# Optimization experiments

Measured on AMD Instinct MI355X. Metric: run time of the kernel, lower is better.

## Reference

```python
import jax, jax.numpy as jnp
import numpy as np

B, T, C, H = 2, 64, 384, 768
LR, MOM, DECAY = 0.01, 0.9, 0.001


def pscan(gates, tokens):
    """parallel_scan_log: x[t] = gates[t]*x[t-1] + tokens[t] along axis 1.
    gates [B,S], tokens [B,S,...]."""
    extra = tokens.ndim - gates.ndim
    g = gates.reshape(gates.shape + (1,) * extra)
    g = jnp.clip(g, 1e-7, 1.0 - 1e-7)
    lc = jnp.cumsum(jnp.log(g), axis=1)              # log cumulative gates
    return jnp.exp(lc) * jnp.cumsum(tokens * jnp.exp(-lc), axis=1)


def setup_inputs():
    key = jax.random.key(0)
    ks = jax.random.split(key, 12)
    s = 0.02
    W0 = jax.random.normal(ks[0], (H, C), jnp.float32) * s
    W1 = jax.random.normal(ks[1], (C, H), jnp.float32) * s
    return {
        "x": jax.random.normal(ks[2], (B, T, C), jnp.float32),
        "Wq": jax.random.normal(ks[3], (C, C), jnp.float32) * s, "bq": jnp.zeros((C,), jnp.float32),
        "Wk": jax.random.normal(ks[4], (C, C), jnp.float32) * s, "bk": jnp.zeros((C,), jnp.float32),
        "Wv": jax.random.normal(ks[5], (C, C), jnp.float32) * s, "bv": jnp.zeros((C,), jnp.float32),
        "Wo": jax.random.normal(ks[6], (C, C), jnp.float32) * s, "bo": jnp.zeros((C,), jnp.float32),
        "init_query": jax.random.normal(ks[7], (1, 1, C), jnp.float32) * s,
        "sW0": jnp.broadcast_to(W0, (B, H, C)) + 0.0,
        "sb0": jnp.zeros((B, H), jnp.float32),
        "sW1": jnp.broadcast_to(W1, (B, C, H)) + 0.0,
        "sb1": jnp.zeros((B, C), jnp.float32),
    }


def reference(x, Wq, bq, Wk, bk, Wv, bv, Wo, bo, init_query, sW0, sb0, sW1, sb1):
    dt = x.dtype
    # ---- retrieval (causal: uses init_query since no previous segment) ----
    q = jnp.broadcast_to(init_query, (B, 1, C)) @ Wq.T + bq          # [B,1,C]
    h_pre = jnp.einsum('bqc,bhc->bqh', q, sW0) + sb0[:, None]
    h = h_pre * jax.nn.sigmoid(h_pre)                                 # SiLU
    pred = jnp.einsum('bqh,bch->bqc', h, sW1) + sb1[:, None]
    out = pred @ Wo.T + bo                                            # [B,1,C]

    # ---- test-time memory update: per-token MSE gradients ----
    k = x @ Wk.T + bk                                                 # [B,T,C]
    v = x @ Wv.T + bv
    h1_pre = jnp.einsum('btc,bhc->bth', k, sW0) + sb0[:, None]
    sig = jax.nn.sigmoid(h1_pre)
    h1 = h1_pre * sig
    p = jnp.einsum('bth,bch->btc', h1, sW1) + sb1[:, None]
    dp = p - v                                                        # d(MSE)/d(pred)
    dW1 = jnp.einsum('btc,bth->btch', dp, h1)                         # [B,T,C,H]
    db1 = dp
    dh1 = jnp.einsum('btc,bch->bth', dp, sW1)
    dh1p = dh1 * (sig * (1 + h1_pre * (1 - sig)))                     # SiLU grad
    dW0 = jnp.einsum('bth,btc->bthc', dh1p, k)                        # [B,T,H,C]
    db0 = dh1p

    # ---- momentum scan + decayed weight scan ----
    def update(W, g):
        surprise = -LR * g                                            # [B,T,...]
        m = pscan(jnp.full((B, T), MOM, dt), (1.0 - MOM) * surprise)  # EMA of surprises
        toks = jnp.concatenate([W[:, None], m], axis=1)               # seed with current weight
        gts = jnp.concatenate([jnp.ones((B, 1), dt),
                               jnp.full((B, T), 1.0 - DECAY, dt)], axis=1)
        return pscan(gts, toks)[:, -1]                                # final weight after segment

    nW0 = update(sW0, dW0)
    nb0 = update(sb0, db0)
    nW1 = update(sW1, dW1)
    nb1 = update(sb1, db1)
    return out, nW0, nb0, nW1, nb1
```

## Files before the change

### kernel.cpp

```cpp
#include <hip/hip_runtime.h>
#include <hip/hip_bf16.h>
#include <cmath>

#define BB 2
#define TT 64
#define CC 384
#define HH 768

#define O_OUT 0
#define O_NW0 768
#define O_NB0 (768 + 589824)
#define O_NW1 (O_NB0 + 1536)
#define O_NB1 (O_NW1 + 589824)

#define GRID_BLKS 312
#define BAR_MAGIC 0x5F3A9D71u
#define AGT __HIP_MEMORY_SCOPE_AGENT

#define W_ARRX(w, x) (32 + ((w) * 8 + (x)) * 32)
#define W_WBD(w)     (1056 + (w) * 32)
#define W_DONE(w)    (1184 + (w) * 32)
#define W_DEP        1312
#define W_NJAN       1344
#define W_CLAIM      1376
#define BAR_WORDS    1536

struct Coefs { float ct[TT]; float dfac; };

typedef __attribute__((ext_vector_type(8))) short bf16x8;
typedef __attribute__((ext_vector_type(4))) float f32x4;

__device__ __forceinline__ float bf2f(unsigned short u) {
    union { unsigned int i; float f; } x; x.i = ((unsigned int)u) << 16; return x.f;
}
__device__ __forceinline__ unsigned short f2bf(float f) {
    union { float f; unsigned int i; } u; u.f = f;
    unsigned int x = u.i;
    unsigned int r = (x + 0x7fffu + ((x >> 16) & 1u)) >> 16;
    return (unsigned short)r;
}
__device__ __forceinline__ f32x4 mfma16(bf16x8 a, bf16x8 b, f32x4 c) {
    return __builtin_amdgcn_mfma_f32_16x16x32_bf16(a, b, c, 0, 0, 0);
}
__device__ __forceinline__ bf16x8 ldbf8(const unsigned short* p) {
    return *(const bf16x8*)p;
}
__device__ __forceinline__ bf16x8 ldcvt8(const float* p) {
    float4 a = *(const float4*)p, b = *(const float4*)(p + 4);
    bf16x8 r;
    r[0] = (short)f2bf(a.x); r[1] = (short)f2bf(a.y); r[2] = (short)f2bf(a.z); r[3] = (short)f2bf(a.w);
    r[4] = (short)f2bf(b.x); r[5] = (short)f2bf(b.y); r[6] = (short)f2bf(b.z); r[7] = (short)f2bf(b.w);
    return r;
}

__device__ __forceinline__ unsigned aload(unsigned* p) {
    return __hip_atomic_load(p, __ATOMIC_RELAXED, AGT);
}
__device__ __forceinline__ void aadd(unsigned* p, unsigned v) {
    __hip_atomic_fetch_add(p, v, __ATOMIC_RELAXED, AGT);
}
__device__ __forceinline__ void astore(unsigned* p, unsigned v) {
    __hip_atomic_store(p, v, __ATOMIC_RELAXED, AGT);
}
__device__ __forceinline__ void bar_reset(unsigned* bar) {
    for (int i = 0; i < 32; ++i) astore(bar + 32 + i * 32, 0u);
    for (int w = 0; w < 4; ++w) { astore(bar + W_WBD(w), 0u); astore(bar + W_DONE(w), 0u); }
    astore(bar + W_DEP, 0u);
    astore(bar + W_NJAN, 0u);
    for (int i = 0; i < 8; ++i) astore(bar + W_CLAIM + i, 0u);
}

struct KArgs {
    const float *x, *Wq, *bq, *Wk, *bk, *Wv, *bv, *Wo, *bo, *iq;
    const float *sW0, *sb0, *sW1, *sb1;
    unsigned short *kb_bf, *h1_bf, *dp_bf;
    float *vb, *qb, *hret, *pred, *dsil, *dh1p, *warm;
    unsigned *bar;
    float *out;
    Coefs cf;
};

__device__ __forceinline__ void gsync(unsigned* bar, int w, bool jan, int xcc) {
    __syncthreads();
    if (threadIdx.x == 0) {
        aadd(bar + W_ARRX(w, xcc), 1u);
        if (jan) {
            for (;;) {
                unsigned s = 0;
                #pragma unroll
                for (int x = 0; x < 8; ++x) s += aload(bar + W_ARRX(w, x));
                if (s == GRID_BLKS) break;
                __builtin_amdgcn_s_sleep(2);
            }
            __builtin_amdgcn_fence(__ATOMIC_RELEASE, "agent");
            asm volatile("s_waitcnt vmcnt(0)" ::: "memory");
            aadd(bar + W_WBD(w), 1u);
            unsigned nj = aload(bar + W_NJAN);
            while (aload(bar + W_WBD(w)) < nj) __builtin_amdgcn_s_sleep(2);
            __builtin_amdgcn_fence(__ATOMIC_ACQUIRE, "agent");
            aadd(bar + W_DONE(w), 1u);
        }
        for (;;) {
            unsigned d = aload(bar + W_DONE(w));
            if (d) { unsigned nj = aload(bar + W_NJAN); if (d >= nj) break; }
            __builtin_amdgcn_s_sleep(2);
        }
        if (w == 3) {
            unsigned old = __hip_atomic_fetch_add(bar + W_DEP, 1u, __ATOMIC_RELAXED, AGT);
            if (old == GRID_BLKS - 1) bar_reset(bar);
        }
    }
    __syncthreads();
}

__global__ void __launch_bounds__(256, 2) fused(KArgs A) {
    __shared__ __align__(16) unsigned char sbuf[49920];
    const int blk = blockIdx.x, j = threadIdx.x;

    bool jan = false; int xcc = 0;
    if (j == 0) {
        if (blk == 0) {
            if (aload(A.bar) != BAR_MAGIC) {
                bar_reset(A.bar);
                __hip_atomic_store(A.bar, BAR_MAGIC, __ATOMIC_RELEASE, AGT);
            }
        } else {
            while (aload(A.bar) != BAR_MAGIC) __builtin_amdgcn_s_sleep(1);
        }
        asm volatile("s_getreg_b32 %0, hwreg(HW_REG_XCC_ID)" : "=s"(xcc));
        xcc &= 7;
        unsigned prev = atomicCAS(A.bar + W_CLAIM + xcc, 0u, (unsigned)(blk + 1));
        if (prev == 0) {
            jan = true;
            aadd(A.bar + W_NJAN, 1u);
            asm volatile("s_waitcnt vmcnt(0)" ::: "memory");
        }
    }

    if (blk < 51) {
        const int wid = j >> 6, L = j & 63;
        const int w = blk * 4 + wid;
        const int lrow = L & 15, kq = (L >> 4) * 8, quad = L >> 4;
        int mf, npair;
        if (w < 192) { mf = w % 8; npair = w / 8; }
        else         { mf = 8;     npair = 24 + (w - 192); }
        const float* Arow = (mf < 8) ? (A.x + (size_t)(mf * 16 + lrow) * CC) : A.iq;
        const int n0 = npair * 32 + lrow, n1 = n0 + 16;
        const float* B0 = (n0 < CC) ? (A.Wk + (size_t)n0 * CC)
                        : (n0 < 2 * CC) ? (A.Wv + (size_t)(n0 - CC) * CC)
                        : (A.Wq + (size_t)(n0 - 2 * CC) * CC);
        const float* B1 = (n1 < CC) ? (A.Wk + (size_t)n1 * CC)
                        : (n1 < 2 * CC) ? (A.Wv + (size_t)(n1 - CC) * CC)
                        : (A.Wq + (size_t)(n1 - 2 * CC) * CC);
        f32x4 acc0 = {0,0,0,0}, acc1 = {0,0,0,0};
        #pragma unroll 2
        for (int s = 0; s < CC / 32; ++s) {
            int k = s * 32 + kq;
            bf16x8 a = ldcvt8(Arow + k);
            bf16x8 b0 = ldcvt8(B0 + k), b1 = ldcvt8(B1 + k);
            acc0 = mfma16(a, b0, acc0); acc1 = mfma16(a, b1, acc1);
        }
        #pragma unroll
        for (int ni = 0; ni < 2; ++ni) {
            f32x4 acc = ni == 0 ? acc0 : acc1;
            int n = npair * 32 + ni * 16 + lrow;
            if (mf < 8) {
                #pragma unroll
                for (int r = 0; r < 4; ++r) {
                    int m = mf * 16 + quad * 4 + r;
                    float v = acc[r];
                    if (n < CC) A.kb_bf[(size_t)m * CC + n] = f2bf(v + A.bk[n]);
                    else        A.vb[(size_t)m * CC + (n - CC)] = v + A.bv[n - CC];
                }
            } else if (quad == 0) {
                A.qb[n - 2 * CC] = acc[0] + A.bq[n - 2 * CC];
            }
        }
    } else {
        int t = (blk - 51) * 256 + j;
        float acc = 0.f;
        for (int g = t; g < 331776; g += (GRID_BLKS - 51) * 256) {
            const float4* src; int off;
            if      (g < 147456) { src = (const float4*)A.sW0; off = g; }
            else if (g < 294912) { src = (const float4*)A.sW1; off = g - 147456; }
            else                 { src = (const float4*)A.Wo;  off = g - 294912; }
            float4 v = src[off];
            acc += v.x + v.y + v.z + v.w;
        }
        if (acc != acc) A.warm[0] = acc;
    }

    gsync(A.bar, 0, jan, xcc);

    if (blk < 60) {
        const int b = blk / 30;
        const int wid = j >> 6, L = j & 63;
        const int w = (blk % 30) * 4 + wid;
        const int mf = w % 5, npair = w / 5;
        const int lrow = L & 15, kq = (L >> 4) * 8, quad = L >> 4;
        const unsigned short* Abf = A.kb_bf + (size_t)(b * TT + mf * 16 + lrow) * CC;
        const int n0 = npair * 32 + lrow;
        const float* B0 = A.sW0 + (size_t)(b * HH + n0) * CC;
        const float* B1 = B0 + 16 * CC;
        f32x4 acc0 = {0,0,0,0}, acc1 = {0,0,0,0};
        if (mf < 4) {
            #pragma unroll 2
            for (int s = 0; s < CC / 32; ++s) {
                int k = s * 32 + kq;
                bf16x8 a = ldbf8(Abf + k);
                bf16x8 b0 = ldcvt8(B0 + k), b1 = ldcvt8(B1 + k);
                acc0 = mfma16(a, b0, acc0); acc1 = mfma16(a, b1, acc1);
            }
        } else {
            #pragma unroll 2
            for (int s = 0; s < CC / 32; ++s) {
                int k = s * 32 + kq;
                bf16x8 a = ldcvt8(A.qb + k);
                bf16x8 b0 = ldcvt8(B0 + k), b1 = ldcvt8(B1 + k);
                acc0 = mfma16(a, b0, acc0); acc1 = mfma16(a, b1, acc1);
            }
        }
        #pragma unroll
        for (int ni = 0; ni < 2; ++ni) {
            f32x4 acc = ni == 0 ? acc0 : acc1;
            int n = npair * 32 + ni * 16 + lrow;
            float bias = A.sb0[b * HH + n];
            if (mf < 4) {
                #pragma unroll
                for (int r = 0; r < 4; ++r) {
                    int t = mf * 16 + quad * 4 + r;
                    float pre = acc[r] + bias;
                    float sig = 1.f / (1.f + expf(-pre));
                    size_t idx = (size_t)(b * TT + t) * HH + n;
                    A.h1_bf[idx] = f2bf(pre * sig);
                    A.dsil[idx]  = sig * (1.f + pre * (1.f - sig));
                }
            } else if (quad == 0) {
                float pre = acc[0] + bias;
                float sig = 1.f / (1.f + expf(-pre));
                A.hret[b * HH + n] = pre * sig;
            }
        }
    }

    gsync(A.bar, 1, jan, xcc);

    if (blk < 30) {
        const int b = blk / 15;
        const int wid = j >> 6, L = j & 63;
        const int w = (blk % 15) * 4 + wid;
        const int mf = w % 5, npair = w / 5;
        const int lrow = L & 15, kq = (L >> 4) * 8, quad = L >> 4;
        const unsigned short* Abf = A.h1_bf + (size_t)(b * TT + mf * 16 + lrow) * HH;
        const float* Aq = A.hret + (size_t)b * HH;
        const int n0 = npair * 32 + lrow;
        const float* B0 = A.sW1 + (size_t)(b * CC + n0) * HH;
        const float* B1 = B0 + 16 * HH;
        f32x4 acc0 = {0,0,0,0}, acc1 = {0,0,0,0};
        if (mf < 4) {
            #pragma unroll 2
            for (int s = 0; s < HH / 32; ++s) {
                int k = s * 32 + kq;
                bf16x8 a = ldbf8(Abf + k);
                bf16x8 b0 = ldcvt8(B0 + k), b1 = ldcvt8(B1 + k);
                acc0 = mfma16(a, b0, acc0); acc1 = mfma16(a, b1, acc1);
            }
        } else {
            #pragma unroll 2
            for (int s = 0; s < HH / 32; ++s) {
                int k = s * 32 + kq;
                bf16x8 a = ldcvt8(Aq + k);
                bf16x8 b0 = ldcvt8(B0 + k), b1 = ldcvt8(B1 + k);
                acc0 = mfma16(a, b0, acc0); acc1 = mfma16(a, b1, acc1);
            }
        }
        #pragma unroll
        for (int ni = 0; ni < 2; ++ni) {
            f32x4 acc = ni == 0 ? acc0 : acc1;
            int n = npair * 32 + ni * 16 + lrow;
            float bias = A.sb1[b * CC + n];
            if (mf < 4) {
                #pragma unroll
                for (int r = 0; r < 4; ++r) {
                    int t = mf * 16 + quad * 4 + r;
                    size_t idx = (size_t)(b * TT + t) * CC + n;
                    A.dp_bf[idx] = f2bf(acc[r] + bias - A.vb[idx]);
                }
            } else if (quad == 0) {
                A.pred[b * CC + n] = acc[0] + bias;
            }
        }
    }

    gsync(A.bar, 2, jan, xcc);

    if (blk < 48) {
        unsigned short* ldsT = (unsigned short*)sbuf;
        const int b = blk / 24, h0 = (blk % 24) * 32;
        {
            const int hl = j & 31, cs = j >> 5;
            const float* base = A.sW1 + (size_t)b * CC * HH + h0 + hl;
            for (int c = cs; c < CC; c += 8)
                ldsT[c * 33 + hl] = f2bf(base[(size_t)c * HH]);
        }
        __syncthreads();
        const int wid = j >> 6, L = j & 63;
        const int lrow = L & 15, kq = (L >> 4) * 8, quad = L >> 4;
        const unsigned short* Abf = A.dp_bf + (size_t)(b * TT + wid * 16 + lrow) * CC;
        f32x4 acc0 = {0,0,0,0}, acc1 = {0,0,0,0};
        for (int s = 0; s < CC / 32; ++s) {
            int k = s * 32 + kq;
            bf16x8 a = ldbf8(Abf + k);
            bf16x8 b0, b1;
            #pragma unroll
            for (int i = 0; i < 8; ++i) {
                b0[i] = (short)ldsT[(k + i) * 33 + lrow];
                b1[i] = (short)ldsT[(k + i) * 33 + 16 + lrow];
            }
            acc0 = mfma16(a, b0, acc0); acc1 = mfma16(a, b1, acc1);
        }
        #pragma unroll
        for (int ni = 0; ni < 2; ++ni) {
            f32x4 acc = ni == 0 ? acc0 : acc1;
            int hl = ni * 16 + lrow;
            #pragma unroll
            for (int r = 0; r < 4; ++r) {
                int t = wid * 16 + quad * 4 + r;
                float ds = A.dsil[(size_t)(b * TT + t) * HH + h0 + hl];
                A.dh1p[(size_t)(b * TT + t) * HH + h0 + hl] = A.cf.ct[t] * (acc[r] * ds);
            }
        }
    } else if (blk < 96) {
        float* vecs = (float*)sbuf;
        float* part = (float*)(sbuf + 4096);
        const int rb = blk - 48;
        const int b = rb / 24, nt = rb % 24;
        if (j < CC / 4) ((float4*)vecs)[j] = ((const float4*)(A.pred + b * CC))[j];
        __syncthreads();
        const int nl = j & 15, ks = j >> 4;
        const int n = nt * 16 + nl;
        const float4* wr = (const float4*)(A.Wo + (size_t)n * CC + ks * 24);
        float s = 0.f;
        #pragma unroll
        for (int i = 0; i < 6; ++i) {
            float4 a4 = wr[i];
            const float* v = vecs + ks * 24 + i * 4;
            s += a4.x * v[0] + a4.y * v[1] + a4.z * v[2] + a4.w * v[3];
        }
        part[ks * 17 + nl] = s;
        __syncthreads();
        if (j < 16) {
            int n2 = nt * 16 + j;
            float acc = A.bo[n2];
            #pragma unroll
            for (int kk = 0; kk < 16; ++kk) acc += part[kk * 17 + j];
            A.out[O_OUT + b * CC + n2] = acc;
        }
    }

    gsync(A.bar, 3, jan, xcc);

    for (int tile = blk; tile < 576; tile += GRID_BLKS) {
        __syncthreads();
        if (tile < 288) {
            float* a_t = (float*)sbuf;
            float* e_t = (float*)(sbuf + 8192);
            const int b = tile / 144, rem = tile % 144;
            const int c0 = (rem / 12) * 32, h0 = (rem % 12) * 64;
            for (int i = j; i < TT * 32; i += 256) {
                int t = i >> 5, c = i & 31;
                a_t[t * 32 + c] = A.cf.ct[t] * bf2f(A.dp_bf[((size_t)(b * TT + t)) * CC + c0 + c]);
            }
            for (int i = j; i < TT * 64; i += 256) {
                int t = i >> 6, h = i & 63;
                e_t[t * 64 + h] = bf2f(A.h1_bf[((size_t)(b * TT + t)) * HH + h0 + h]);
            }
            __syncthreads();
            const int ci = j & 31, hb = (j >> 5) * 8;
            float acc[8] = {0, 0, 0, 0, 0, 0, 0, 0};
            for (int t = 0; t < TT; ++t) {
                float av = a_t[t * 32 + ci];
                #pragma unroll
                for (int m = 0; m < 8; ++m) acc[m] += av * e_t[t * 64 + hb + m];
            }
            const size_t idx = ((size_t)b * CC + c0 + ci) * HH + h0 + hb;
            const float4* w4 = (const float4*)(A.sW1 + idx);
            float4 wa = w4[0], wb = w4[1];
            float4 o0, o1;
            o0.x = A.cf.dfac * wa.x - acc[0]; o0.y = A.cf.dfac * wa.y - acc[1];
            o0.z = A.cf.dfac * wa.z - acc[2]; o0.w = A.cf.dfac * wa.w - acc[3];
            o1.x = A.cf.dfac * wb.x - acc[4]; o1.y = A.cf.dfac * wb.y - acc[5];
            o1.z = A.cf.dfac * wb.z - acc[6]; o1.w = A.cf.dfac * wb.w - acc[7];
            *(float4*)(A.out + O_NW1 + idx) = o0;
            *(float4*)(A.out + O_NW1 + idx + 4) = o1;
            if (h0 == 0 && j < 32) {
                float s = 0.f;
                for (int t = 0; t < TT; ++t) s += a_t[t * 32 + j];
                A.out[O_NB1 + b * CC + c0 + j] = A.cf.dfac * A.sb1[b * CC + c0 + j] - s;
            }
        } else {
            float* a_t = (float*)sbuf;
            float* e_t = (float*)(sbuf + 8192);
            const int u = tile - 288;
            const int b = u / 144, rem = u % 144;
            const int h0 = (rem / 6) * 32, c0 = (rem % 6) * 64;
            for (int i = j; i < TT * 32; i += 256) {
                int t = i >> 5, hl = i & 31;
                a_t[t * 32 + hl] = A.dh1p[((size_t)(b * TT + t)) * HH + h0 + hl];
            }
            for (int i = j; i < TT * 64; i += 256) {
                int t = i >> 6, c = i & 63;
                e_t[t * 64 + c] = bf2f(A.kb_bf[((size_t)(b * TT + t)) * CC + c0 + c]);
            }
            __syncthreads();
            const int hi = j & 31, cb = (j >> 5) * 8;
            float acc[8] = {0, 0, 0, 0, 0, 0, 0, 0};
            for (int t = 0; t < TT; ++t) {
                float av = a_t[t * 32 + hi];
                #pragma unroll
                for (int m = 0; m < 8; ++m) acc[m] += av * e_t[t * 64 + cb + m];
            }
            const size_t idx = ((size_t)b * HH + h0 + hi) * CC + c0 + cb;
            const float4* w4 = (const float4*)(A.sW0 + idx);
            float4 wa = w4[0], wb = w4[1];
            float4 o0, o1;
            o0.x = A.cf.dfac * wa.x - acc[0]; o0.y = A.cf.dfac * wa.y - acc[1];
            o0.z = A.cf.dfac * wa.z - acc[2]; o0.w = A.cf.dfac * wa.w - acc[3];
            o1.x = A.cf.dfac * wb.x - acc[4]; o1.y = A.cf.dfac * wb.y - acc[5];
            o1.z = A.cf.dfac * wb.z - acc[6]; o1.w = A.cf.dfac * wb.w - acc[7];
            *(float4*)(A.out + O_NW0 + idx) = o0;
            *(float4*)(A.out + O_NW0 + idx + 4) = o1;
            if (c0 == 0 && j < 32) {
                float s = 0.f;
                for (int t = 0; t < TT; ++t) s += a_t[t * 32 + j];
                A.out[O_NB0 + b * HH + h0 + j] = A.cf.dfac * A.sb0[b * HH + h0 + j] - s;
            }
        }
    }
}

extern "C" void kernel_launch(void* const* d_in, const int* in_sizes, int n_in,
                              void* d_out, int out_size, void* d_ws, size_t ws_size,
                              hipStream_t stream) {
    KArgs a;
    a.x   = (const float*)d_in[0];
    a.Wq  = (const float*)d_in[1];
    a.bq  = (const float*)d_in[2];
    a.Wk  = (const float*)d_in[3];
    a.bk  = (const float*)d_in[4];
    a.Wv  = (const float*)d_in[5];
    a.bv  = (const float*)d_in[6];
    a.Wo  = (const float*)d_in[7];
    a.bo  = (const float*)d_in[8];
    a.iq  = (const float*)d_in[9];
    a.sW0 = (const float*)d_in[10];
    a.sb0 = (const float*)d_in[11];
    a.sW1 = (const float*)d_in[12];
    a.sb1 = (const float*)d_in[13];

    a.bar  = (unsigned*)d_ws;
    float* fw = (float*)d_ws + BAR_WORDS;
    a.qb   = fw;
    a.hret = a.qb + 384;
    a.pred = a.hret + 1536;
    a.vb   = a.pred + 768;
    a.dsil = a.vb + 49152;
    a.warm = a.dsil + 98304;
    unsigned short* us = (unsigned short*)(a.warm + 4);
    a.kb_bf = us;
    a.h1_bf = a.kb_bf + 49152;
    a.dp_bf = a.h1_bf + 98304;
    a.dh1p  = (float*)(a.dp_bf + 49152);

    a.out = (float*)d_out;

    const double mom = 0.9, decay = 1.0 - 0.001, lr = 0.01;
    for (int s = 0; s < TT; ++s) {
        double sum = 0.0;
        for (int t = s; t < TT; ++t) sum += pow(decay, (double)(TT - 1 - t)) * pow(mom, (double)(t - s));
        a.cf.ct[s] = (float)(lr * (1.0 - mom) * sum);
    }
    a.cf.dfac = (float)pow(decay, (double)TT);

    fused<<<dim3(GRID_BLKS), dim3(256), 0, stream>>>(a);
}
```

Before: 155.9 us.

## Simplify grid barrier, store intermediates as fp32 with system-scope stores, overlap nW1 tiles

Replaces the per-XCC janitor grid barrier with a flat 8-shard arrival counter that every block polls. Intermediates (k, h1, dp) are now kept in fp32 and written with system-scope relaxed atomic stores instead of bf16 plain stores, which makes the consumers' bf16 conversion happen at load time. Idle blocks in stage 3 start nW1 outer-product tiles early, leaving fewer tiles after the last barrier, and LDS use is shrunk. The fp32 intermediates double traffic, and every block polling all shards could add contention.

Measured after the change: 162.4 us. 4.1% more time.

```diff
diff --git a/kernel.cpp b/kernel.cpp
--- a/kernel.cpp
+++ b/kernel.cpp
@@ -17,22 +17,15 @@
 #define BAR_MAGIC 0x5F3A9D71u
 #define AGT __HIP_MEMORY_SCOPE_AGENT
 
-#define W_ARRX(w, x) (32 + ((w) * 8 + (x)) * 32)
-#define W_WBD(w)     (1056 + (w) * 32)
-#define W_DONE(w)    (1184 + (w) * 32)
-#define W_DEP        1312
-#define W_NJAN       1344
-#define W_CLAIM      1376
-#define BAR_WORDS    1536
+#define W_ARR(w, s) (32 + ((w) * 8 + (s)) * 32)
+#define W_DEP       (32 + 32 * 32)
+#define BAR_WORDS   1536
 
 struct Coefs { float ct[TT]; float dfac; };
 
 typedef __attribute__((ext_vector_type(8))) short bf16x8;
 typedef __attribute__((ext_vector_type(4))) float f32x4;
 
-__device__ __forceinline__ float bf2f(unsigned short u) {
-    union { unsigned int i; float f; } x; x.i = ((unsigned int)u) << 16; return x.f;
-}
 __device__ __forceinline__ unsigned short f2bf(float f) {
     union { float f; unsigned int i; } u; u.f = f;
     unsigned int x = u.i;
@@ -41,9 +34,6 @@
 }
 __device__ __forceinline__ f32x4 mfma16(bf16x8 a, bf16x8 b, f32x4 c) {
     return __builtin_amdgcn_mfma_f32_16x16x32_bf16(a, b, c, 0, 0, 0);
-}
-__device__ __forceinline__ bf16x8 ldbf8(const unsigned short* p) {
-    return *(const bf16x8*)p;
 }
 __device__ __forceinline__ bf16x8 ldcvt8(const float* p) {
     float4 a = *(const float4*)p, b = *(const float4*)(p + 4);
@@ -53,6 +43,9 @@
     return r;
 }
 
+__device__ __forceinline__ void sysst(float* p, float v) {
+    __hip_atomic_store(p, v, __ATOMIC_RELAXED, __HIP_MEMORY_SCOPE_SYSTEM);
+}
 __device__ __forceinline__ unsigned aload(unsigned* p) {
     return __hip_atomic_load(p, __ATOMIC_RELAXED, AGT);
 }
@@ -64,45 +57,31 @@
 }
 __device__ __forceinline__ void bar_reset(unsigned* bar) {
     for (int i = 0; i < 32; ++i) astore(bar + 32 + i * 32, 0u);
-    for (int w = 0; w < 4; ++w) { astore(bar + W_WBD(w), 0u); astore(bar + W_DONE(w), 0u); }
     astore(bar + W_DEP, 0u);
-    astore(bar + W_NJAN, 0u);
-    for (int i = 0; i < 8; ++i) astore(bar + W_CLAIM + i, 0u);
 }
 
 struct KArgs {
     const float *x, *Wq, *bq, *Wk, *bk, *Wv, *bv, *Wo, *bo, *iq;
     const float *sW0, *sb0, *sW1, *sb1;
-    unsigned short *kb_bf, *h1_bf, *dp_bf;
+    float *kb, *h1, *dp;
     float *vb, *qb, *hret, *pred, *dsil, *dh1p, *warm;
     unsigned *bar;
     float *out;
     Coefs cf;
 };
 
-__device__ __forceinline__ void gsync(unsigned* bar, int w, bool jan, int xcc) {
+__device__ __forceinline__ void gsync(unsigned* bar, int w, int shard) {
     __syncthreads();
     if (threadIdx.x == 0) {
-        aadd(bar + W_ARRX(w, xcc), 1u);
-        if (jan) {
-            for (;;) {
-                unsigned s = 0;
-                #pragma unroll
-                for (int x = 0; x < 8; ++x) s += aload(bar + W_ARRX(w, x));
-                if (s == GRID_BLKS) break;
-                __builtin_amdgcn_s_sleep(2);
-            }
-            __builtin_amdgcn_fence(__ATOMIC_RELEASE, "agent");
-            asm volatile("s_waitcnt vmcnt(0)" ::: "memory");
-            aadd(bar + W_WBD(w), 1u);
-            unsigned nj = aload(bar + W_NJAN);
-            while (aload(bar + W_WBD(w)) < nj) __builtin_amdgcn_s_sleep(2);
-            __builtin_amdgcn_fence(__ATOMIC_ACQUIRE, "agent");
-            aadd(bar + W_DONE(w), 1u);
-        }
+        if (w == 0) {
+            while (aload(bar) != BAR_MAGIC) __builtin_amdgcn_s_sleep(1);
+        }
+        aadd(bar + W_ARR(w, shard), 1u);
         for (;;) {
-            unsigned d = aload(bar + W_DONE(w));
-            if (d) { unsigned nj = aload(bar + W_NJAN); if (d >= nj) break; }
+            unsigned s = 0;
+            #pragma unroll
+            for (int x = 0; x < 8; ++x) s += aload(bar + W_ARR(w, x));
+            if (s == GRID_BLKS) break;
             __builtin_amdgcn_s_sleep(2);
         }
         if (w == 3) {
@@ -113,27 +92,92 @@
     __syncthreads();
 }
 
+__device__ __forceinline__ void nw1_tile(const KArgs& A, unsigned char* sbuf, int tile, int j) {
+    float* a_t = (float*)sbuf;
+    float* e_t = (float*)(sbuf + 8192);
+    const int b = tile / 144, rem = tile % 144;
+    const int c0 = (rem / 12) * 32, h0 = (rem % 12) * 64;
+    for (int i = j; i < TT * 32; i += 256) {
+        int t = i >> 5, c = i & 31;
+        a_t[t * 32 + c] = A.cf.ct[t] * A.dp[((size_t)(b * TT + t)) * CC + c0 + c];
+    }
+    for (int i = j; i < TT * 64; i += 256) {
+        int t = i >> 6, h = i & 63;
+        e_t[t * 64 + h] = A.h1[((size_t)(b * TT + t)) * HH + h0 + h];
+    }
+    __syncthreads();
+    const int ci = j & 31, hb = (j >> 5) * 8;
+    float acc[8] = {0, 0, 0, 0, 0, 0, 0, 0};
+    for (int t = 0; t < TT; ++t) {
+        float av = a_t[t * 32 + ci];
+        #pragma unroll
+        for (int m = 0; m < 8; ++m) acc[m] += av * e_t[t * 64 + hb + m];
+    }
+    const size_t idx = ((size_t)b * CC + c0 + ci) * HH + h0 + hb;
+    const float4* w4 = (const float4*)(A.sW1 + idx);
+    float4 wa = w4[0], wb = w4[1];
+    float4 o0, o1;
+    o0.x = A.cf.dfac * wa.x - acc[0]; o0.y = A.cf.dfac * wa.y - acc[1];
+    o0.z = A.cf.dfac * wa.z - acc[2]; o0.w = A.cf.dfac * wa.w - acc[3];
+    o1.x = A.cf.dfac * wb.x - acc[4]; o1.y = A.cf.dfac * wb.y - acc[5];
+    o1.z = A.cf.dfac * wb.z - acc[6]; o1.w = A.cf.dfac * wb.w - acc[7];
+    *(float4*)(A.out + O_NW1 + idx) = o0;
+    *(float4*)(A.out + O_NW1 + idx + 4) = o1;
+    if (h0 == 0 && j < 32) {
+        float s = 0.f;
+        for (int t = 0; t < TT; ++t) s += a_t[t * 32 + j];
+        A.out[O_NB1 + b * CC + c0 + j] = A.cf.dfac * A.sb1[b * CC + c0 + j] - s;
+    }
+}
+
+__device__ __forceinline__ void nw0_tile(const KArgs& A, unsigned char* sbuf, int tile, int j) {
+    float* a_t = (float*)sbuf;
+    float* e_t = (float*)(sbuf + 8192);
+    const int b = tile / 144, rem = tile % 144;
+    const int h0 = (rem / 6) * 32, c0 = (rem % 6) * 64;
+    for (int i = j; i < TT * 32; i += 256) {
+        int t = i >> 5, hl = i & 31;
+        a_t[t * 32 + hl] = A.dh1p[((size_t)(b * TT + t)) * HH + h0 + hl];
+    }
+    for (int i = j; i < TT * 64; i += 256) {
+        int t = i >> 6, c = i & 63;
+        e_t[t * 64 + c] = A.kb[((size_t)(b * TT + t)) * CC + c0 + c];
+    }
+    __syncthreads();
+    const int hi = j & 31, cb = (j >> 5) * 8;
+    float acc[8] = {0, 0, 0, 0, 0, 0, 0, 0};
+    for (int t = 0; t < TT; ++t) {
+        float av = a_t[t * 32 + hi];
+        #pragma unroll
+        for (int m = 0; m < 8; ++m) acc[m] += av * e_t[t * 64 + cb + m];
+    }
+    const size_t idx = ((size_t)b * HH + h0 + hi) * CC + c0 + cb;
+    const float4* w4 = (const float4*)(A.sW0 + idx);
+    float4 wa = w4[0], wb = w4[1];
+    float4 o0, o1;
+    o0.x = A.cf.dfac * wa.x - acc[0]; o0.y = A.cf.dfac * wa.y - acc[1];
+    o0.z = A.cf.dfac * wa.z - acc[2]; o0.w = A.cf.dfac * wa.w - acc[3];
+    o1.x = A.cf.dfac * wb.x - acc[4]; o1.y = A.cf.dfac * wb.y - acc[5];
+    o1.z = A.cf.dfac * wb.z - acc[6]; o1.w = A.cf.dfac * wb.w - acc[7];
+    *(float4*)(A.out + O_NW0 + idx) = o0;
+    *(float4*)(A.out + O_NW0 + idx + 4) = o1;
+    if (c0 == 0 && j < 32) {
+        float s = 0.f;
+        for (int t = 0; t < TT; ++t) s += a_t[t * 32 + j];
+        A.out[O_NB0 + b * HH + h0 + j] = A.cf.dfac * A.sb0[b * HH + h0 + j] - s;
+    }
+}
+
 __global__ void __launch_bounds__(256, 2) fused(KArgs A) {
-    __shared__ __align__(16) unsigned char sbuf[49920];
+    __shared__ __align__(16) unsigned char sbuf[25344];
     const int blk = blockIdx.x, j = threadIdx.x;
-
-    bool jan = false; int xcc = 0;
-    if (j == 0) {
-        if (blk == 0) {
-            if (aload(A.bar) != BAR_MAGIC) {
-                bar_reset(A.bar);
-                __hip_atomic_store(A.bar, BAR_MAGIC, __ATOMIC_RELEASE, AGT);
-            }
-        } else {
-            while (aload(A.bar) != BAR_MAGIC) __builtin_amdgcn_s_sleep(1);
-        }
-        asm volatile("s_getreg_b32 %0, hwreg(HW_REG_XCC_ID)" : "=s"(xcc));
-        xcc &= 7;
-        unsigned prev = atomicCAS(A.bar + W_CLAIM + xcc, 0u, (unsigned)(blk + 1));
-        if (prev == 0) {
-            jan = true;
-            aadd(A.bar + W_NJAN, 1u);
+    const int shard = blk & 7;
+
+    if (blk == 0 && j == 0) {
+        if (aload(A.bar) != BAR_MAGIC) {
+            bar_reset(A.bar);
             asm volatile("s_waitcnt vmcnt(0)" ::: "memory");
+            astore(A.bar, BAR_MAGIC);
         }
     }
 
@@ -169,11 +213,11 @@
                 for (int r = 0; r < 4; ++r) {
                     int m = mf * 16 + quad * 4 + r;
                     float v = acc[r];
-                    if (n < CC) A.kb_bf[(size_t)m * CC + n] = f2bf(v + A.bk[n]);
-                    else        A.vb[(size_t)m * CC + (n - CC)] = v + A.bv[n - CC];
+                    if (n < CC) sysst(&A.kb[(size_t)m * CC + n], v + A.bk[n]);
+                    else        sysst(&A.vb[(size_t)m * CC + (n - CC)], v + A.bv[n - CC]);
                 }
             } else if (quad == 0) {
-                A.qb[n - 2 * CC] = acc[0] + A.bq[n - 2 * CC];
+                sysst(&A.qb[n - 2 * CC], acc[0] + A.bq[n - 2 * CC]);
             }
         }
     } else {
@@ -190,7 +234,7 @@
         if (acc != acc) A.warm[0] = acc;
     }
 
-    gsync(A.bar, 0, jan, xcc);
+    gsync(A.bar, 0, shard);
 
     if (blk < 60) {
         const int b = blk / 30;
@@ -198,27 +242,17 @@
         const int w = (blk % 30) * 4 + wid;
         const int mf = w % 5, npair = w / 5;
         const int lrow = L & 15, kq = (L >> 4) * 8, quad = L >> 4;
-        const unsigned short* Abf = A.kb_bf + (size_t)(b * TT + mf * 16 + lrow) * CC;
+        const float* Arow = (mf < 4) ? (A.kb + (size_t)(b * TT + mf * 16 + lrow) * CC) : A.qb;
         const int n0 = npair * 32 + lrow;
         const float* B0 = A.sW0 + (size_t)(b * HH + n0) * CC;
         const float* B1 = B0 + 16 * CC;
         f32x4 acc0 = {0,0,0,0}, acc1 = {0,0,0,0};
-        if (mf < 4) {
-            #pragma unroll 2
-            for (int s = 0; s < CC / 32; ++s) {
-                int k = s * 32 + kq;
-                bf16x8 a = ldbf8(Abf + k);
-                bf16x8 b0 = ldcvt8(B0 + k), b1 = ldcvt8(B1 + k);
-                acc0 = mfma16(a, b0, acc0); acc1 = mfma16(a, b1, acc1);
-            }
-        } else {
-            #pragma unroll 2
-            for (int s = 0; s < CC / 32; ++s) {
-                int k = s * 32 + kq;
-                bf16x8 a = ldcvt8(A.qb + k);
-                bf16x8 b0 = ldcvt8(B0 + k), b1 = ldcvt8(B1 + k);
-                acc0 = mfma16(a, b0, acc0); acc1 = mfma16(a, b1, acc1);
-            }
+        #pragma unroll 2
+        for (int s = 0; s < CC / 32; ++s) {
+            int k = s * 32 + kq;
+            bf16x8 a = ldcvt8(Arow + k);
+            bf16x8 b0 = ldcvt8(B0 + k), b1 = ldcvt8(B1 + k);
+            acc0 = mfma16(a, b0, acc0); acc1 = mfma16(a, b1, acc1);
         }
         #pragma unroll
         for (int ni = 0; ni < 2; ++ni) {
@@ -232,18 +266,18 @@
                     float pre = acc[r] + bias;
                     float sig = 1.f / (1.f + expf(-pre));
                     size_t idx = (size_t)(b * TT + t) * HH + n;
-                    A.h1_bf[idx] = f2bf(pre * sig);
-                    A.dsil[idx]  = sig * (1.f + pre * (1.f - sig));
+                    sysst(&A.h1[idx], pre * sig);
+                    sysst(&A.dsil[idx], sig * (1.f + pre * (1.f - sig)));
                 }
             } else if (quad == 0) {
                 float pre = acc[0] + bias;
                 float sig = 1.f / (1.f + expf(-pre));
-                A.hret[b * HH + n] = pre * sig;
+                sysst(&A.hret[b * HH + n], pre * sig);
             }
         }
     }
 
-    gsync(A.bar, 1, jan, xcc);
+    gsync(A.bar, 1, shard);
 
     if (blk < 30) {
         const int b = blk / 15;
@@ -251,28 +285,18 @@
         const int w = (blk % 15) * 4 + wid;
         const int mf = w % 5, npair = w / 5;
         const int lrow = L & 15, kq = (L >> 4) * 8, quad = L >> 4;
-        const unsigned short* Abf = A.h1_bf + (size_t)(b * TT + mf * 16 + lrow) * HH;
-        const float* Aq = A.hret + (size_t)b * HH;
+        const float* Arow = (mf < 4) ? (A.h1 + (size_t)(b * TT + mf * 16 + lrow) * HH)
+                                     : (A.hret + (size_t)b * HH);
         const int n0 = npair * 32 + lrow;
         const float* B0 = A.sW1 + (size_t)(b * CC + n0) * HH;
         const float* B1 = B0 + 16 * HH;
         f32x4 acc0 = {0,0,0,0}, acc1 = {0,0,0,0};
-        if (mf < 4) {
-            #pragma unroll 2
-            for (int s = 0; s < HH / 32; ++s) {
-                int k = s * 32 + kq;
-                bf16x8 a = ldbf8(Abf + k);
-                bf16x8 b0 = ldcvt8(B0 + k), b1 = ldcvt8(B1 + k);
-                acc0 = mfma16(a, b0, acc0); acc1 = mfma16(a, b1, acc1);
-            }
-        } else {
-            #pragma unroll 2
-            for (int s = 0; s < HH / 32; ++s) {
-                int k = s * 32 + kq;
-                bf16x8 a = ldcvt8(Aq + k);
-                bf16x8 b0 = ldcvt8(B0 + k), b1 = ldcvt8(B1 + k);
-                acc0 = mfma16(a, b0, acc0); acc1 = mfma16(a, b1, acc1);
-            }
+        #pragma unroll 2
+        for (int s = 0; s < HH / 32; ++s) {
+            int k = s * 32 + kq;
+            bf16x8 a = ldcvt8(Arow + k);
+            bf16x8 b0 = ldcvt8(B0 + k), b1 = ldcvt8(B1 + k);
+            acc0 = mfma16(a, b0, acc0); acc1 = mfma16(a, b1, acc1);
         }
         #pragma unroll
         for (int ni = 0; ni < 2; ++ni) {
@@ -284,15 +308,15 @@
                 for (int r = 0; r < 4; ++r) {
                     int t = mf * 16 + quad * 4 + r;
                     size_t idx = (size_t)(b * TT + t) * CC + n;
-                    A.dp_bf[idx] = f2bf(acc[r] + bias - A.vb[idx]);
+                    sysst(&A.dp[idx], acc[r] + bias - A.vb[idx]);
                 }
             } else if (quad == 0) {
-                A.pred[b * CC + n] = acc[0] + bias;
+                sysst(&A.pred[b * CC + n], acc[0] + bias);
             }
         }
     }
 
-    gsync(A.bar, 2, jan, xcc);
+    gsync(A.bar, 2, shard);
 
     if (blk < 48) {
         unsigned short* ldsT = (unsigned short*)sbuf;
@@ -306,11 +330,11 @@
         __syncthreads();
         const int wid = j >> 6, L = j & 63;
         const int lrow = L & 15, kq = (L >> 4) * 8, quad = L >> 4;
-        const unsigned short* Abf = A.dp_bf + (size_t)(b * TT + wid * 16 + lrow) * CC;
+        const float* Arow = A.dp + (size_t)(b * TT + wid * 16 + lrow) * CC;
         f32x4 acc0 = {0,0,0,0}, acc1 = {0,0,0,0};
         for (int s = 0; s < CC / 32; ++s) {
             int k = s * 32 + kq;
-            bf16x8 a = ldbf8(Abf + k);
+            bf16x8 a = ldcvt8(Arow + k);
             bf16x8 b0, b1;
             #pragma unroll
             for (int i = 0; i < 8; ++i) {
@@ -327,7 +351,7 @@
             for (int r = 0; r < 4; ++r) {
                 int t = wid * 16 + quad * 4 + r;
                 float ds = A.dsil[(size_t)(b * TT + t) * HH + h0 + hl];
-                A.dh1p[(size_t)(b * TT + t) * HH + h0 + hl] = A.cf.ct[t] * (acc[r] * ds);
+                sysst(&A.dh1p[(size_t)(b * TT + t) * HH + h0 + hl], A.cf.ct[t] * (acc[r] * ds));
             }
         }
     } else if (blk < 96) {
@@ -356,86 +380,18 @@
             for (int kk = 0; kk < 16; ++kk) acc += part[kk * 17 + j];
             A.out[O_OUT + b * CC + n2] = acc;
         }
-    }
-
-    gsync(A.bar, 3, jan, xcc);
-
-    for (int tile = blk; tile < 576; tile += GRID_BLKS) {
+    } else {
+        nw1_tile(A, sbuf, blk - 96, j);
+    }
+
+    gsync(A.bar, 3, shard);
+
+    for (int pass = 0; pass < 2; ++pass) {
+        int td = blk + pass * GRID_BLKS;
+        if (td >= 360) break;
         __syncthreads();
-        if (tile < 288) {
-            float* a_t = (float*)sbuf;
-            float* e_t = (float*)(sbuf + 8192);
-            const int b = tile / 144, rem = tile % 144;
-            const int c0 = (rem / 12) * 32, h0 = (rem % 12) * 64;
-            for (int i = j; i < TT * 32; i += 256) {
-                int t = i >> 5, c = i & 31;
-                a_t[t * 32 + c] = A.cf.ct[t] * bf2f(A.dp_bf[((size_t)(b * TT + t)) * CC + c0 + c]);
-            }
-            for (int i = j; i < TT * 64; i += 256) {
-                int t = i >> 6, h = i & 63;
-                e_t[t * 64 + h] = bf2f(A.h1_bf[((size_t)(b * TT + t)) * HH + h0 + h]);
-            }
-            __syncthreads();
-            const int ci = j & 31, hb = (j >> 5) * 8;
-            float acc[8] = {0, 0, 0, 0, 0, 0, 0, 0};
-            for (int t = 0; t < TT; ++t) {
-                float av = a_t[t * 32 + ci];
-                #pragma unroll
-                for (int m = 0; m < 8; ++m) acc[m] += av * e_t[t * 64 + hb + m];
-            }
-            const size_t idx = ((size_t)b * CC + c0 + ci) * HH + h0 + hb;
-            const float4* w4 = (const float4*)(A.sW1 + idx);
-            float4 wa = w4[0], wb = w4[1];
-            float4 o0, o1;
-            o0.x = A.cf.dfac * wa.x - acc[0]; o0.y = A.cf.dfac * wa.y - acc[1];
-            o0.z = A.cf.dfac * wa.z - acc[2]; o0.w = A.cf.dfac * wa.w - acc[3];
-            o1.x = A.cf.dfac * wb.x - acc[4]; o1.y = A.cf.dfac * wb.y - acc[5];
-            o1.z = A.cf.dfac * wb.z - acc[6]; o1.w = A.cf.dfac * wb.w - acc[7];
-            *(float4*)(A.out + O_NW1 + idx) = o0;
-            *(float4*)(A.out + O_NW1 + idx + 4) = o1;
-            if (h0 == 0 && j < 32) {
-                float s = 0.f;
-                for (int t = 0; t < TT; ++t) s += a_t[t * 32 + j];
-                A.out[O_NB1 + b * CC + c0 + j] = A.cf.dfac * A.sb1[b * CC + c0 + j] - s;
-            }
-        } else {
-            float* a_t = (float*)sbuf;
-            float* e_t = (float*)(sbuf + 8192);
-            const int u = tile - 288;
-            const int b = u / 144, rem = u % 144;
-            const int h0 = (rem / 6) * 32, c0 = (rem % 6) * 64;
-            for (int i = j; i < TT * 32; i += 256) {
-                int t = i >> 5, hl = i & 31;
-                a_t[t * 32 + hl] = A.dh1p[((size_t)(b * TT + t)) * HH + h0 + hl];
-            }
-            for (int i = j; i < TT * 64; i += 256) {
-                int t = i >> 6, c = i & 63;
-                e_t[t * 64 + c] = bf2f(A.kb_bf[((size_t)(b * TT + t)) * CC + c0 + c]);
-            }
-            __syncthreads();
-            const int hi = j & 31, cb = (j >> 5) * 8;
-            float acc[8] = {0, 0, 0, 0, 0, 0, 0, 0};
-            for (int t = 0; t < TT; ++t) {
-                float av = a_t[t * 32 + hi];
-                #pragma unroll
-                for (int m = 0; m < 8; ++m) acc[m] += av * e_t[t * 64 + cb + m];
-            }
-            const size_t idx = ((size_t)b * HH + h0 + hi) * CC + c0 + cb;
-            const float4* w4 = (const float4*)(A.sW0 + idx);
-            float4 wa = w4[0], wb = w4[1];
-            float4 o0, o1;
-            o0.x = A.cf.dfac * wa.x - acc[0]; o0.y = A.cf.dfac * wa.y - acc[1];
-            o0.z = A.cf.dfac * wa.z - acc[2]; o0.w = A.cf.dfac * wa.w - acc[3];
-            o1.x = A.cf.dfac * wb.x - acc[4]; o1.y = A.cf.dfac * wb.y - acc[5];
-            o1.z = A.cf.dfac * wb.z - acc[6]; o1.w = A.cf.dfac * wb.w - acc[7];
-            *(float4*)(A.out + O_NW0 + idx) = o0;
-            *(float4*)(A.out + O_NW0 + idx + 4) = o1;
-            if (c0 == 0 && j < 32) {
-                float s = 0.f;
-                for (int t = 0; t < TT; ++t) s += a_t[t * 32 + j];
-                A.out[O_NB0 + b * HH + h0 + j] = A.cf.dfac * A.sb0[b * HH + h0 + j] - s;
-            }
-        }
+        if (td < 72) nw1_tile(A, sbuf, 216 + td, j);
+        else         nw0_tile(A, sbuf, td - 72, j);
     }
 }
 
@@ -466,11 +422,10 @@
     a.vb   = a.pred + 768;
     a.dsil = a.vb + 49152;
     a.warm = a.dsil + 98304;
-    unsigned short* us = (unsigned short*)(a.warm + 4);
-    a.kb_bf = us;
-    a.h1_bf = a.kb_bf + 49152;
-    a.dp_bf = a.h1_bf + 98304;
-    a.dh1p  = (float*)(a.dp_bf + 49152);
+    a.kb   = a.warm + 4;
+    a.h1   = a.kb + 49152;
+    a.dp   = a.h1 + 98304;
+    a.dh1p = a.dp + 49152;
 
     a.out = (float*)d_out;
 
```
